# Optimization experiments

Measured on AMD Instinct MI355X. Metric: run time of the kernel, lower is better.

Reference implementation:

```python
import jax, jax.numpy as jnp
import numpy as np

K_EDE = 10.0   # self.k
T_EDE = 0.1    # self.t
BN_EPS = 1e-5
T_A = 576.0    # 3*3*64, hardcoded in my_bn1/my_bn2


def qfn(x, prec):
    # dorefa-style round quantizer with straight-through gradient
    n = float(2 ** prec - 1)
    return x + jax.lax.stop_gradient(jnp.round(x * n) / n - x)


@jax.custom_vjp
def binary_quantize(x):
    return jnp.sign(x)


def _bq_fwd(x):
    return jnp.sign(x), x


def _bq_bwd(x, g):
    # IR-Net EDE backward: k * t * (1 - tanh(x*t)^2)
    return (K_EDE * T_EDE * (1.0 - jnp.tanh(x * T_EDE) ** 2) * g,)


binary_quantize.defvjp(_bq_fwd, _bq_bwd)


def _clip_T(x):
    T = jnp.maximum(jnp.abs(x.min()), jnp.abs(x.max()))
    return jax.lax.stop_gradient(jnp.clip(T, 1e-10, 255.0))


def quantize_conv_act(x, prec):
    # my_quantize_conv: clamp to [-T, T], scale to [-1,1], qfn (no rescale by T)
    T = _clip_T(x)
    return qfn(jnp.clip(x, -T, T) / T, prec)


def quantize(x, prec):
    # my_quantize: same but rescaled back by T
    T = _clip_T(x)
    return qfn(jnp.clip(x, -T, T) / T, prec) * T


def ir_conv2d(a, w, stride):
    # IR-Net 1w8a IRConv2d: per-out-channel normalize, binarize (sign), power-of-2 scale
    co = w.shape[0]
    wf = w.reshape(co, -1)
    bw = (w - wf.mean(1)[:, None, None, None]) / jnp.std(wf, axis=1, ddof=1)[:, None, None, None]
    sw = jax.lax.stop_gradient(
        2.0 ** jnp.round(jnp.log2(jnp.abs(bw.reshape(co, -1)).mean(1)))
    )[:, None, None, None]
    bw = binary_quantize(bw) * sw
    return jax.lax.conv_general_dilated(
        a, bw, window_strides=(stride, stride), padding=[(1, 1), (1, 1)],
        dimension_numbers=('NCHW', 'OIHW', 'NCHW'))


def bn_as_quantized_affine(x, gamma, beta, mean, var):
    # my_bn1/my_bn2 (eval mode): BN folded into per-channel scale+bias.
    # The original builds a CxC diagonal 1x1 conv; since off-diagonal entries are 0,
    # both the quantization stats (max|.|) and the conv reduce exactly to this
    # per-channel affine, which is the faithful fused form.
    std = jnp.sqrt(var + BN_EPS)
    w = gamma / std
    b = beta - w * mean
    qw = quantize(w, 3)
    qb = quantize(b, 12)
    aq = qfn(x / T_A, 10) * T_A  # my_quantize_activation(input, 10, T_a)
    return aq * qw[None, :, None, None] + qb[None, :, None, None]


def _block(x, w1, w2, g1, b1, m1, v1, g2, b2, m2, v2):
    xq = quantize_conv_act(x, 3)
    out = ir_conv2d(xq, w1, 1)
    out = bn_as_quantized_affine(out, g1, b1, m1, v1) + xq  # identity shortcut
    out = jnp.clip(out, -1.0, 1.0)  # hardtanh
    x1 = quantize_conv_act(out, 3)
    out = ir_conv2d(x1, w2, 1)
    out = bn_as_quantized_affine(out, g2, b2, m2, v2) + x1
    return jnp.clip(out, -1.0, 1.0)


def setup_inputs() -> dict:
    key = jax.random.key(0)
    ks = jax.random.split(key, 11)
    B, C, H, W = 128, 64, 56, 56
    return {
        'x': jax.random.normal(ks[0], (B, C, H, W), jnp.float32),
        'w1': jax.random.normal(ks[1], (C, C, 3, 3), jnp.float32) * 0.1,
        'w2': jax.random.normal(ks[2], (C, C, 3, 3), jnp.float32) * 0.1,
        'g1': jax.random.uniform(ks[3], (C,), jnp.float32, 0.5, 1.5),
        'b1': jax.random.normal(ks[4], (C,), jnp.float32) * 0.1,
        'm1': jax.random.normal(ks[5], (C,), jnp.float32) * 0.1,
        'v1': jax.random.uniform(ks[6], (C,), jnp.float32, 0.5, 1.5),
        'g2': jax.random.uniform(ks[7], (C,), jnp.float32, 0.5, 1.5),
        'b2': jax.random.normal(ks[8], (C,), jnp.float32) * 0.1,
        'm2': jax.random.normal(ks[9], (C,), jnp.float32) * 0.1,
        'v2': jax.random.uniform(ks[10], (C,), jnp.float32, 0.5, 1.5),
    }


def reference(x, w1, w2, g1, b1, m1, v1, g2, b2, m2, v2):
    return _block(x, w1, w2, g1, b1, m1, v1, g2, b2, m2, v2)
```

## Files before the change

### kernel.cpp

```cpp
#include <hip/hip_runtime.h>
#include <stdint.h>

typedef int v4i   __attribute__((ext_vector_type(4)));
typedef int v16i  __attribute__((ext_vector_type(16)));

#define B_    128
#define C_    64
#define H_    56
#define W_    56
#define HW_   3136
#define NELEM (B_*C_*HW_)

#define OFF_K0   0
#define OFF_K1   ((size_t)NELEM)
#define OFF_WB   ((size_t)2*NELEM)
#define OFF_PAR  (OFF_WB + 2*4*9*64*16)
#define OFF_MAX  (OFF_PAR + 1536)

__global__ void k_absmax(const float* __restrict__ x, unsigned* __restrict__ maxbits) {
    __shared__ float smax[4];
    const int n4 = NELEM / 4;
    const int stride = gridDim.x * blockDim.x;
    int i = blockIdx.x * blockDim.x + threadIdx.x;
    float ma = 0.f, mb = 0.f;
    for (; i + stride < n4; i += 2 * stride) {
        float4 va = ((const float4*)x)[i];
        float4 vb = ((const float4*)x)[i + stride];
        ma = fmaxf(ma, fmaxf(fmaxf(fabsf(va.x), fabsf(va.y)), fmaxf(fabsf(va.z), fabsf(va.w))));
        mb = fmaxf(mb, fmaxf(fmaxf(fabsf(vb.x), fabsf(vb.y)), fmaxf(fabsf(vb.z), fabsf(vb.w))));
    }
    if (i < n4) {
        float4 va = ((const float4*)x)[i];
        ma = fmaxf(ma, fmaxf(fmaxf(fabsf(va.x), fabsf(va.y)), fmaxf(fabsf(va.z), fabsf(va.w))));
    }
    float m = fmaxf(ma, mb);
    for (int off = 32; off; off >>= 1) m = fmaxf(m, __shfl_down(m, off, 64));
    if ((threadIdx.x & 63) == 0) smax[threadIdx.x >> 6] = m;
    __syncthreads();
    if (threadIdx.x == 0) {
        float mm = fmaxf(fmaxf(smax[0], smax[1]), fmaxf(smax[2], smax[3]));
        atomicMax(maxbits, __float_as_uint(mm));
    }
}

__global__ __launch_bounds__(256) void k_quant(const float* __restrict__ x,
                                               const unsigned* __restrict__ maxbits,
                                               int8_t* __restrict__ k8) {
    __shared__ unsigned tword[64 * 112];
    const int n  = blockIdx.x / 7;
    const int y8 = (blockIdx.x % 7) * 8;
    const float T = fminf(fmaxf(__uint_as_float(*maxbits), 1e-10f), 255.0f);
    const float* xb = x + (size_t)n * 64 * HW_ + y8 * 56;
#pragma unroll
    for (int it = 0; it < 28; it++) {
        const int flat = it * 256 + threadIdx.x;
        const int c = flat / 112, u = flat - c * 112;
        float4 v = *(const float4*)(xb + (size_t)c * HW_ + u * 4);
        float vv[4] = {v.x, v.y, v.z, v.w};
        unsigned pack = 0;
#pragma unroll
        for (int q = 0; q < 4; q++) {
            float t = fminf(fmaxf(vv[q], -T), T);
            float uq = __fdiv_rn(t, T);
            int k = (int)rintf(__fmul_rn(uq, 7.0f));
            pack |= ((unsigned)k & 0xFFu) << (8 * q);
        }
        tword[c * 112 + u] = pack;
    }
    __syncthreads();
#pragma unroll
    for (int it = 0; it < 7; it++) {
        const int w = it * 256 + threadIdx.x;
        const int rg = w / 56, xx = w - rg * 56;
        const int r = rg >> 2, g = rg & 3;
        const int sh = (xx & 3) * 8;
        const int ub = r * 14 + (xx >> 2);
        unsigned b[4];
#pragma unroll
        for (int q = 0; q < 4; q++) {
            unsigned acc = 0;
#pragma unroll
            for (int c2 = 0; c2 < 4; c2++) {
                unsigned byte = (tword[(g * 16 + q * 4 + c2) * 112 + ub] >> sh) & 0xFFu;
                acc |= byte << (8 * c2);
            }
            b[q] = acc;
        }
        int4 outv; outv.x = (int)b[0]; outv.y = (int)b[1]; outv.z = (int)b[2]; outv.w = (int)b[3];
        *(int4*)(k8 + ((((size_t)(n * 56 + y8 + r)) * 4 + g) * 56 + xx) * 16) = outv;
    }
}

__device__ __forceinline__ float pw_reduce64(float r) {
    r = __fadd_rn(r, __shfl_xor(r, 1, 64));
    r = __fadd_rn(r, __shfl_xor(r, 2, 64));
    r = __fadd_rn(r, __shfl_xor(r, 4, 64));
    r = __fadd_rn(r, __shfl_xor(r, 8, 64));
    r = __fadd_rn(r, __shfl_xor(r, 16, 64));
    r = __fadd_rn(r, __shfl_xor(r, 32, 64));
    return r;
}

__global__ void k_prepw(const float* __restrict__ w1, const float* __restrict__ w2,
                        int8_t* __restrict__ wb, float* __restrict__ par) {
    const int layer = blockIdx.x >> 6;
    const int co    = blockIdx.x & 63;
    const float* w = (layer ? w2 : w1) + (size_t)co * 576;
    const int lane = threadIdx.x;
    const int base = (lane >> 3) * 72 + (lane & 7);

    float v[9];
#pragma unroll
    for (int i = 0; i < 9; i++) v[i] = w[base + 8 * i];

    float s = v[0];
#pragma unroll
    for (int i = 1; i < 9; i++) s = __fadd_rn(s, v[i]);
    const float mean = __fdiv_rn(pw_reduce64(s), 576.0f);

    float d0 = __fsub_rn(v[0], mean);
    float sq = __fmul_rn(d0, d0);
#pragma unroll
    for (int i = 1; i < 9; i++) {
        float d = __fsub_rn(v[i], mean);
        sq = __fadd_rn(sq, __fmul_rn(d, d));
    }
    const float sig = __fsqrt_rn(__fdiv_rn(pw_reduce64(sq), 575.0f));

    float sa = fabsf(__fdiv_rn(__fsub_rn(v[0], mean), sig));
#pragma unroll
    for (int i = 1; i < 9; i++)
        sa = __fadd_rn(sa, fabsf(__fdiv_rn(__fsub_rn(v[i], mean), sig)));
    const float ma = __fdiv_rn(pw_reduce64(sa), 576.0f);
    const float p  = rintf(log2f(ma));
    if (lane == 0) par[256 + layer * 64 + co] = __fdiv_rn(exp2f(p), 7.0f);

#pragma unroll
    for (int i = 0; i < 9; i++) {
        int ig = base + 8 * i;
        float d = __fsub_rn(v[i], mean);
        int8_t sg = (d > 0.0f) ? (int8_t)1 : ((d < 0.0f) ? (int8_t)-1 : (int8_t)0);
        int ci = ig / 9, t = ig % 9;
        wb[((((size_t)layer * 4 + (ci >> 4)) * 9 + t) * 64 + co) * 16 + (ci & 15)] = sg;
    }
}

__global__ void k_prepbn(const float* g1, const float* bb1, const float* mm1, const float* vv1,
                         const float* g2, const float* bb2, const float* mm2, const float* vv2,
                         float* __restrict__ par) {
    const int layer = threadIdx.x >> 6;
    const int c = threadIdx.x & 63;
    const float* g  = layer ? g2  : g1;
    const float* be = layer ? bb2 : bb1;
    const float* mu = layer ? mm2 : mm1;
    const float* va = layer ? vv2 : vv1;
    const float stdv = __fsqrt_rn(__fadd_rn(va[c], 1e-5f));
    const float w = __fdiv_rn(g[c], stdv);
    const float b = __fsub_rn(be[c], __fmul_rn(w, mu[c]));
    float aw = fabsf(w), ab = fabsf(b);
    for (int off = 32; off; off >>= 1) {
        aw = fmaxf(aw, __shfl_xor(aw, off, 64));
        ab = fmaxf(ab, __shfl_xor(ab, off, 64));
    }
    const float Tw = fminf(fmaxf(aw, 1e-10f), 255.0f);
    const float Tb = fminf(fmaxf(ab, 1e-10f), 255.0f);
    {
        float vq = __fdiv_rn(fminf(fmaxf(w, -Tw), Tw), Tw);
        float r  = rintf(__fmul_rn(vq, 7.0f));
        float qf = __fadd_rn(vq, __fsub_rn(__fdiv_rn(r, 7.0f), vq));
        par[layer * 64 + c] = __fmul_rn(qf, Tw);
    }
    {
        float vq = __fdiv_rn(fminf(fmaxf(b, -Tb), Tb), Tb);
        float r  = rintf(__fmul_rn(vq, 4095.0f));
        float qf = __fadd_rn(vq, __fsub_rn(__fdiv_rn(r, 4095.0f), vq));
        par[128 + layer * 64 + c] = __fmul_rn(qf, Tb);
    }
}

template <int LAYER>
__global__ __launch_bounds__(256) void k_conv(const int8_t* __restrict__ kin,
                                              const int8_t* __restrict__ wb,
                                              const float* __restrict__ par,
                                              int8_t* __restrict__ kout,
                                              float* __restrict__ fout) {
    __shared__ __align__(16) int8_t halo[4 * 4 * 58 * 16];
    __shared__ __align__(16) int8_t wsm[4 * 9 * 64 * 16];
    __shared__ float xqlut[16];
    const int n  = blockIdx.x / 28;
    const int y0 = (blockIdx.x % 28) * 2;
    const int tid = threadIdx.x;

    for (int u = tid; u < 928; u += 256) {
        int xx = u % 58, gr = u / 58;
        int g = gr >> 2, r = gr & 3;
        int y = y0 - 1 + r, xg = xx - 1;
        int4 val = {0, 0, 0, 0};
        if ((unsigned)y < 56u && (unsigned)xg < 56u)
            val = *(const int4*)(kin + ((((size_t)(n * 56 + y)) * 4 + g) * 56 + xg) * 16);
        *(int4*)(halo + ((g * 4 + r) * 58 + xx) * 16) = val;
    }
    const int8_t* wsrc = wb + (size_t)(LAYER - 1) * 36864;
    for (int u = tid; u < 2304; u += 256)
        *(int4*)(wsm + u * 16) = *(const int4*)(wsrc + u * 16);
    if (tid < 15) xqlut[tid] = __fdiv_rn((float)(tid - 7), 7.0f);
    __syncthreads();

    const int wv = tid >> 6, lane = tid & 63;
    const int ml = lane & 31, khalf = lane >> 5;
    const int mbase = wv * 32;

    const int m = mbase + ml;
    const int m_eff = (m < 112) ? m : 111;
    const int rm = m_eff / 56, cm = m_eff % 56;

    v16i acc0, acc1;
#pragma unroll
    for (int i = 0; i < 16; i++) { acc0[i] = 0; acc1[i] = 0; }

#pragma unroll
    for (int s = 0; s < 9; s++) {
        const int ky = s / 3, kx = s % 3;
#pragma unroll
        for (int kb = 0; kb < 2; kb++) {
            const int g = kb * 2 + khalf;
            v4i a  = *(const v4i*)(halo + ((g * 4 + rm + ky) * 58 + cm + kx) * 16);
            v4i b0 = *(const v4i*)(wsm + ((g * 9 + s) * 64 + ml) * 16);
            v4i b1 = *(const v4i*)(wsm + ((g * 9 + s) * 64 + ml + 32) * 16);
            if (LAYER == 1) {
                acc0 = __builtin_amdgcn_mfma_i32_32x32x32_i8(a, b0, acc0, 0, 0, 0);
                acc1 = __builtin_amdgcn_mfma_i32_32x32x32_i8(a, b1, acc1, 0, 0, 0);
            } else {
                acc0 = __builtin_amdgcn_mfma_i32_32x32x32_i8(b0, a, acc0, 0, 0, 0);
                acc1 = __builtin_amdgcn_mfma_i32_32x32x32_i8(b1, a, acc1, 0, 0, 0);
            }
        }
    }

    const float* qw = par + (LAYER - 1) * 64;
    const float* qb = par + 128 + (LAYER - 1) * 64;
    const float* sc = par + 256 + (LAYER - 1) * 64;

    if (LAYER == 1) {
#pragma unroll
        for (int t = 0; t < 2; t++) {
            const int co = ml + 32 * t;
            const float qwf = qw[co], qbf = qb[co], scf = sc[co];
#pragma unroll
            for (int r = 0; r < 16; r++) {
                const int mrow = mbase + 4 * khalf + (r & 3) + 8 * (r >> 2);
                if (mrow >= 112) continue;
                const float Sf = (float)(t ? acc1[r] : acc0[r]);
                float convf = __fmul_rn(Sf, scf);
                float xb = __fdiv_rn(convf, 576.0f);
                float rr = rintf(__fmul_rn(xb, 1023.0f));
                float q1 = __fdiv_rn(rr, 1023.0f);
                float y1 = __fadd_rn(xb, __fsub_rn(q1, xb));
                float aq = __fmul_rn(y1, 576.0f);
                const int rloc = mrow / 56, cloc = mrow % 56;
                const int kc = (int)halo[(((co >> 4) * 4 + rloc + 1) * 58 + cloc + 1) * 16 + (co & 15)];
                const float xq = xqlut[kc + 7];
                float val = __fadd_rn(__fadd_rn(__fmul_rn(aq, qwf), qbf), xq);
                val = fminf(fmaxf(val, -1.0f), 1.0f);
                const int k2 = (int)rintf(__fmul_rn(val, 7.0f));
                kout[((((size_t)(n * 56 + y0 + rloc)) * 4 + (co >> 4)) * 56 + cloc) * 16 + (co & 15)]
                    = (int8_t)k2;
            }
        }
    } else {
        int kcw[16];
        {
            const int4* hp = (const int4*)halo;
#pragma unroll
            for (int g = 0; g < 4; g++) {
                int4 chunk = hp[(g * 4 + rm + 1) * 58 + cm + 1];
                kcw[g * 4 + 0] = chunk.x; kcw[g * 4 + 1] = chunk.y;
                kcw[g * 4 + 2] = chunk.z; kcw[g * 4 + 3] = chunk.w;
            }
        }
        float* fn = fout + (size_t)n * 64 * HW_ + (size_t)(y0 + rm) * 56 + cm;
        const bool mok = (m < 112);
#pragma unroll
        for (int t = 0; t < 2; t++) {
#pragma unroll
            for (int r = 0; r < 16; r++) {
                const int co = (r & 3) + 8 * (r >> 2) + 4 * khalf + 32 * t;
                const float qwf = qw[co], qbf = qb[co], scf = sc[co];
                const float Sf = (float)(t ? acc1[r] : acc0[r]);
                float convf = __fmul_rn(Sf, scf);
                float xb = __fdiv_rn(convf, 576.0f);
                float rr = rintf(__fmul_rn(xb, 1023.0f));
                float q1 = __fdiv_rn(rr, 1023.0f);
                float y1 = __fadd_rn(xb, __fsub_rn(q1, xb));
                float aq = __fmul_rn(y1, 576.0f);
                const int kc = (int)(int8_t)(kcw[co >> 2] >> ((co & 3) * 8));
                const float xq = xqlut[kc + 7];
                float val = __fadd_rn(__fadd_rn(__fmul_rn(aq, qwf), qbf), xq);
                val = fminf(fmaxf(val, -1.0f), 1.0f);
                if (mok) fn[(size_t)co * HW_] = val;
            }
        }
    }
}

extern "C" void kernel_launch(void* const* d_in, const int* in_sizes, int n_in,
                              void* d_out, int out_size, void* d_ws, size_t ws_size,
                              hipStream_t stream) {
    const float* x  = (const float*)d_in[0];
    const float* w1 = (const float*)d_in[1];
    const float* w2 = (const float*)d_in[2];
    const float* g1 = (const float*)d_in[3];
    const float* b1 = (const float*)d_in[4];
    const float* m1 = (const float*)d_in[5];
    const float* v1 = (const float*)d_in[6];
    const float* g2 = (const float*)d_in[7];
    const float* b2 = (const float*)d_in[8];
    const float* m2 = (const float*)d_in[9];
    const float* v2 = (const float*)d_in[10];

    char* ws = (char*)d_ws;
    int8_t*  k0  = (int8_t*)(ws + OFF_K0);
    int8_t*  k1  = (int8_t*)(ws + OFF_K1);
    int8_t*  wbp = (int8_t*)(ws + OFF_WB);
    float*   par = (float*)(ws + OFF_PAR);
    unsigned* mx = (unsigned*)(ws + OFF_MAX);

    hipMemsetAsync(mx, 0, 4, stream);
    k_absmax<<<2048, 256, 0, stream>>>(x, mx);
    k_quant<<<B_ * 7, 256, 0, stream>>>(x, mx, k0);
    k_prepw<<<128, 64, 0, stream>>>(w1, w2, wbp, par);
    k_prepbn<<<1, 128, 0, stream>>>(g1, b1, m1, v1, g2, b2, m2, v2, par);
    k_conv<1><<<B_ * 28, 256, 0, stream>>>(k0, wbp, par, k1, nullptr);
    k_conv<2><<<B_ * 28, 256, 0, stream>>>(k1, wbp, par, nullptr, (float*)d_out);
}
```

Baseline: 352.6 us.

## Replace float epilogue quantization chain with integer-rounded lookup; halve k_quant tile

The conv epilogue now computes the 10-bit activation level directly as rint(S*K) in double, with a per-channel constant K folding the weight scale, /7, /576 and *1023. The dequantized value comes from a shared-memory lookup table, replacing the chain of correctly-rounded divides and multiplies. Separately, k_quant now processes 4 rows per block instead of 8, doubling the grid and halving shared memory per block to raise occupancy. The double-precision rounding may differ from the float reference chain at tie points, and the par buffer layout grows to hold doubles.

```diff
diff --git a/kernel.cpp b/kernel.cpp
--- a/kernel.cpp
+++ b/kernel.cpp
@@ -15,7 +15,7 @@
 #define OFF_K1   ((size_t)NELEM)
 #define OFF_WB   ((size_t)2*NELEM)
 #define OFF_PAR  (OFF_WB + 2*4*9*64*16)
-#define OFF_MAX  (OFF_PAR + 1536)
+#define OFF_MAX  (OFF_PAR + 2048)
 
 __global__ void k_absmax(const float* __restrict__ x, unsigned* __restrict__ maxbits) {
     __shared__ float smax[4];
@@ -46,15 +46,15 @@
 __global__ __launch_bounds__(256) void k_quant(const float* __restrict__ x,
                                                const unsigned* __restrict__ maxbits,
                                                int8_t* __restrict__ k8) {
-    __shared__ unsigned tword[64 * 112];
-    const int n  = blockIdx.x / 7;
-    const int y8 = (blockIdx.x % 7) * 8;
+    __shared__ unsigned tword[64 * 56];
+    const int n  = blockIdx.x / 14;
+    const int y4 = (blockIdx.x % 14) * 4;
     const float T = fminf(fmaxf(__uint_as_float(*maxbits), 1e-10f), 255.0f);
-    const float* xb = x + (size_t)n * 64 * HW_ + y8 * 56;
-#pragma unroll
-    for (int it = 0; it < 28; it++) {
+    const float* xb = x + (size_t)n * 64 * HW_ + y4 * 56;
+#pragma unroll
+    for (int it = 0; it < 14; it++) {
         const int flat = it * 256 + threadIdx.x;
-        const int c = flat / 112, u = flat - c * 112;
+        const int c = flat / 56, u = flat - c * 56;
         float4 v = *(const float4*)(xb + (size_t)c * HW_ + u * 4);
         float vv[4] = {v.x, v.y, v.z, v.w};
         unsigned pack = 0;
@@ -65,12 +65,13 @@
             int k = (int)rintf(__fmul_rn(uq, 7.0f));
             pack |= ((unsigned)k & 0xFFu) << (8 * q);
         }
-        tword[c * 112 + u] = pack;
+        tword[c * 56 + u] = pack;
     }
     __syncthreads();
 #pragma unroll
-    for (int it = 0; it < 7; it++) {
+    for (int it = 0; it < 4; it++) {
         const int w = it * 256 + threadIdx.x;
+        if (w >= 896) break;
         const int rg = w / 56, xx = w - rg * 56;
         const int r = rg >> 2, g = rg & 3;
         const int sh = (xx & 3) * 8;
@@ -81,13 +82,13 @@
             unsigned acc = 0;
 #pragma unroll
             for (int c2 = 0; c2 < 4; c2++) {
-                unsigned byte = (tword[(g * 16 + q * 4 + c2) * 112 + ub] >> sh) & 0xFFu;
+                unsigned byte = (tword[(g * 16 + q * 4 + c2) * 56 + ub] >> sh) & 0xFFu;
                 acc |= byte << (8 * c2);
             }
             b[q] = acc;
         }
         int4 outv; outv.x = (int)b[0]; outv.y = (int)b[1]; outv.z = (int)b[2]; outv.w = (int)b[3];
-        *(int4*)(k8 + ((((size_t)(n * 56 + y8 + r)) * 4 + g) * 56 + xx) * 16) = outv;
+        *(int4*)(k8 + ((((size_t)(n * 56 + y4 + r)) * 4 + g) * 56 + xx) * 16) = outv;
     }
 }
 
@@ -133,7 +134,8 @@
         sa = __fadd_rn(sa, fabsf(__fdiv_rn(__fsub_rn(v[i], mean), sig)));
     const float ma = __fdiv_rn(pw_reduce64(sa), 576.0f);
     const float p  = rintf(log2f(ma));
-    if (lane == 0) par[256 + layer * 64 + co] = __fdiv_rn(exp2f(p), 7.0f);
+    if (lane == 0)
+        ((double*)(par + 256))[layer * 64 + co] = exp2((double)p) * (341.0 / 1344.0);
 
 #pragma unroll
     for (int i = 0; i < 9; i++) {
@@ -186,6 +188,7 @@
                                               float* __restrict__ fout) {
     __shared__ __align__(16) int8_t halo[4 * 4 * 58 * 16];
     __shared__ __align__(16) int8_t wsm[4 * 9 * 64 * 16];
+    __shared__ float aql[256];
     __shared__ float xqlut[16];
     const int n  = blockIdx.x / 28;
     const int y0 = (blockIdx.x % 28) * 2;
@@ -203,6 +206,7 @@
     const int8_t* wsrc = wb + (size_t)(LAYER - 1) * 36864;
     for (int u = tid; u < 2304; u += 256)
         *(int4*)(wsm + u * 16) = *(const int4*)(wsrc + u * 16);
+    aql[tid & 255] = __fmul_rn(__fdiv_rn((float)(tid & 255), 1023.0f), 576.0f);
     if (tid < 15) xqlut[tid] = __fdiv_rn((float)(tid - 7), 7.0f);
     __syncthreads();
 
@@ -239,24 +243,24 @@
 
     const float* qw = par + (LAYER - 1) * 64;
     const float* qb = par + 128 + (LAYER - 1) * 64;
-    const float* sc = par + 256 + (LAYER - 1) * 64;
+    const double* Kd = (const double*)(par + 256) + (LAYER - 1) * 64;
 
     if (LAYER == 1) {
 #pragma unroll
         for (int t = 0; t < 2; t++) {
             const int co = ml + 32 * t;
-            const float qwf = qw[co], qbf = qb[co], scf = sc[co];
+            const float qwf = qw[co], qbf = qb[co];
+            const double Kc = Kd[co];
 #pragma unroll
             for (int r = 0; r < 16; r++) {
                 const int mrow = mbase + 4 * khalf + (r & 3) + 8 * (r >> 2);
                 if (mrow >= 112) continue;
-                const float Sf = (float)(t ? acc1[r] : acc0[r]);
-                float convf = __fmul_rn(Sf, scf);
-                float xb = __fdiv_rn(convf, 576.0f);
-                float rr = rintf(__fmul_rn(xb, 1023.0f));
-                float q1 = __fdiv_rn(rr, 1023.0f);
-                float y1 = __fadd_rn(xb, __fsub_rn(q1, xb));
-                float aq = __fmul_rn(y1, 576.0f);
+                const int S = t ? acc1[r] : acc0[r];
+                const int rri = (int)rint((double)S * Kc);
+                const int idx = rri < 0 ? -rri : rri;
+                float aqa = (idx < 256) ? aql[idx]
+                          : __fmul_rn(__fdiv_rn((float)idx, 1023.0f), 576.0f);
+                const float aq = rri < 0 ? -aqa : aqa;
                 const int rloc = mrow / 56, cloc = mrow % 56;
                 const int kc = (int)halo[(((co >> 4) * 4 + rloc + 1) * 58 + cloc + 1) * 16 + (co & 15)];
                 const float xq = xqlut[kc + 7];
@@ -285,14 +289,14 @@
 #pragma unroll
             for (int r = 0; r < 16; r++) {
                 const int co = (r & 3) + 8 * (r >> 2) + 4 * khalf + 32 * t;
-                const float qwf = qw[co], qbf = qb[co], scf = sc[co];
-                const float Sf = (float)(t ? acc1[r] : acc0[r]);
-                float convf = __fmul_rn(Sf, scf);
-                float xb = __fdiv_rn(convf, 576.0f);
-                float rr = rintf(__fmul_rn(xb, 1023.0f));
-                float q1 = __fdiv_rn(rr, 1023.0f);
-                float y1 = __fadd_rn(xb, __fsub_rn(q1, xb));
-                float aq = __fmul_rn(y1, 576.0f);
+                const float qwf = qw[co], qbf = qb[co];
+                const double Kc = Kd[co];
+                const int S = t ? acc1[r] : acc0[r];
+                const int rri = (int)rint((double)S * Kc);
+                const int idx = rri < 0 ? -rri : rri;
+                float aqa = (idx < 256) ? aql[idx]
+                          : __fmul_rn(__fdiv_rn((float)idx, 1023.0f), 576.0f);
+                const float aq = rri < 0 ? -aqa : aqa;
                 const int kc = (int)(int8_t)(kcw[co >> 2] >> ((co & 3) * 8));
                 const float xq = xqlut[kc + 7];
                 float val = __fadd_rn(__fadd_rn(__fmul_rn(aq, qwf), qbf), xq);
@@ -327,7 +331,7 @@
 
     hipMemsetAsync(mx, 0, 4, stream);
     k_absmax<<<2048, 256, 0, stream>>>(x, mx);
-    k_quant<<<B_ * 7, 256, 0, stream>>>(x, mx, k0);
+    k_quant<<<B_ * 14, 256, 0, stream>>>(x, mx, k0);
     k_prepw<<<128, 64, 0, stream>>>(w1, w2, wbp, par);
     k_prepbn<<<1, 128, 0, stream>>>(g1, b1, m1, v1, g2, b2, m2, v2, par);
     k_conv<1><<<B_ * 28, 256, 0, stream>>>(k0, wbp, par, k1, nullptr);
```

Measured after the change: 381.2 us. 8.1% more time.
